# Optimization experiments

Hardware: AMD Instinct MI355X
Metric: run time of the kernel (lower is better)

The kernel has to match this reference:

```python
import jax, jax.numpy as jnp
import numpy as np

BG_CLASS = 3          # eval path drops argmax-class==3
NMS_THRESH = 0.2      # nms(rois, scores, 0.2)
IMG_SIZE = 512.0      # ClipBoxes to 512x512 image
NUM_CLASSES = 4


def _decode_boxes(rois, deltas):
    # BBoxTransform: std weights (0.1, 0.1, 0.2, 0.2), then clip to image
    w = rois[:, 2] - rois[:, 0]
    h = rois[:, 3] - rois[:, 1]
    cx = rois[:, 0] + 0.5 * w
    cy = rois[:, 1] + 0.5 * h
    dx = deltas[:, 0] * 0.1
    dy = deltas[:, 1] * 0.1
    dw = deltas[:, 2] * 0.2
    dh = deltas[:, 3] * 0.2
    pcx = cx + dx * w
    pcy = cy + dy * h
    pw = jnp.exp(dw) * w
    ph = jnp.exp(dh) * h
    boxes = jnp.stack([pcx - 0.5 * pw, pcy - 0.5 * ph,
                       pcx + 0.5 * pw, pcy + 0.5 * ph], axis=1)
    return jnp.clip(boxes, 0.0, IMG_SIZE)


def _iou_one_vs_all(box, boxes):
    x1 = jnp.maximum(box[0], boxes[:, 0])
    y1 = jnp.maximum(box[1], boxes[:, 1])
    x2 = jnp.minimum(box[2], boxes[:, 2])
    y2 = jnp.minimum(box[3], boxes[:, 3])
    inter = jnp.clip(x2 - x1, 0.0) * jnp.clip(y2 - y1, 0.0)
    area_a = (box[2] - box[0]) * (box[3] - box[1])
    area_b = (boxes[:, 2] - boxes[:, 0]) * (boxes[:, 3] - boxes[:, 1])
    return inter / (area_a + area_b - inter + 1e-8)


def _nms_keep_mask(boxes, scores, thresh):
    # Fixed-shape NMS: returns bool keep mask over the original ordering.
    N = boxes.shape[0]
    order = jnp.argsort(-scores)           # descending score
    b = boxes[order]
    idx = jnp.arange(N)

    def body(i, keep):
        iou = _iou_one_vs_all(b[i], b)
        suppress = (iou > thresh) & (idx > i)
        return jnp.where(keep[i], keep & ~suppress, keep)

    keep_sorted = jax.lax.fori_loop(0, N, body, jnp.ones((N,), dtype=bool))
    return jnp.zeros((N,), dtype=bool).at[order].set(keep_sorted)


def _head(f, rois, w6, b6, w7, b7, wc, bc, wr, br):
    # TwoMLPHead
    v = jax.nn.relu(f @ w6.T + b6)          # [N, 1024]
    v = jax.nn.relu(v @ w7.T + b7)          # [N, 1024]
    # FastRCNNPredictor
    c = v @ wc.T + bc                        # [N, num_classes]
    r = v @ wr.T + br                        # [N, num_classes*4]
    classes = jnp.argmax(c, axis=1)          # torch.max(x,1)[1]
    scores = jnp.max(c, axis=1)              # torch.max(x,1)[0]
    deltas = jnp.take_along_axis(r.reshape(-1, NUM_CLASSES, 4),
                                 classes[:, None, None], axis=1)[:, 0, :]
    boxes = _decode_boxes(rois, deltas)
    return scores, classes, boxes


def setup_inputs() -> dict:
    key = jax.random.key(0)
    ks = jax.random.split(key, 10)
    N, D, H = 8000, 12544, 1024
    f = jax.random.normal(ks[0], (N, D), dtype=jnp.float32)
    # valid xyxy ROIs inside 512x512
    xy = jax.random.uniform(ks[1], (N, 2), minval=0.0, maxval=380.0)
    wh = jax.random.uniform(ks[2], (N, 2), minval=20.0, maxval=120.0)
    rois = jnp.concatenate([xy, xy + wh], axis=1).astype(jnp.float32)
    w6 = jax.random.normal(ks[3], (H, D), dtype=jnp.float32) * 0.01
    b6 = jnp.zeros((H,), dtype=jnp.float32)
    w7 = jax.random.normal(ks[4], (H, H), dtype=jnp.float32) * 0.02
    b7 = jnp.zeros((H,), dtype=jnp.float32)
    wc = jax.random.normal(ks[5], (NUM_CLASSES, H), dtype=jnp.float32) * 0.02
    bc = jnp.zeros((NUM_CLASSES,), dtype=jnp.float32)
    wr = jax.random.normal(ks[6], (NUM_CLASSES * 4, H), dtype=jnp.float32) * 0.02
    br = jnp.zeros((NUM_CLASSES * 4,), dtype=jnp.float32)
    return {"f": f, "rois": rois, "w6": w6, "b6": b6, "w7": w7, "b7": b7,
            "wc": wc, "bc": bc, "wr": wr, "br": br}


def reference(f, rois, w6, b6, w7, b7, wc, bc, wr, br):
    scores, classes, boxes = _head(f, rois, w6, b6, w7, b7, wc, bc, wr, br)
    valid = classes != BG_CLASS
    s_masked = jnp.where(valid, scores, -jnp.inf)
    keep = _nms_keep_mask(boxes, s_masked, NMS_THRESH) & valid
    # fixed-shape equivalent of (scores[index], labels[index], bboxes[index])
    return scores, classes, boxes, keep
```

## Files before the change

### kernel.cpp

```cpp
#include <hip/hip_runtime.h>
#include <hip/hip_fp16.h>
#include <math.h>

typedef _Float16 f16;
typedef _Float16 f16x2 __attribute__((ext_vector_type(2)));
typedef _Float16 f16x4 __attribute__((ext_vector_type(4)));
typedef _Float16 f16x8 __attribute__((ext_vector_type(8)));
typedef float f32x4 __attribute__((ext_vector_type(4)));
typedef unsigned long long u64;

#define GLD16(g, s) __builtin_amdgcn_global_load_lds( \
    (const __attribute__((address_space(1))) void*)(g), \
    (__attribute__((address_space(3))) void*)(s), 16, 0, 0)

struct HL { f16 h, l; };
__device__ __forceinline__ HL split1(float e) {
  float em = __uint_as_float(__float_as_uint(e) & 0xFFFFE000u);
  HL r;
  r.h = (f16)em;
  r.l = (f16)(e - em);
  return r;
}

__device__ __forceinline__ void splitcvt8(f32x4 u, f32x4 v, f16x8& H, f16x8& L) {
  union { f16x2 h2[4]; f16x8 h8; } uh, ul;
#pragma unroll
  for (int p = 0; p < 2; ++p) {
    float a = u[2 * p] * 256.0f, b = u[2 * p + 1] * 256.0f;
    float am = __uint_as_float(__float_as_uint(a) & 0xFFFFE000u);
    float bm = __uint_as_float(__float_as_uint(b) & 0xFFFFE000u);
    auto pk = __builtin_amdgcn_cvt_pkrtz(am, bm);
    uh.h2[p] = *reinterpret_cast<f16x2*>(&pk);
    auto pl = __builtin_amdgcn_cvt_pkrtz(a - am, b - bm);
    ul.h2[p] = *reinterpret_cast<f16x2*>(&pl);
  }
#pragma unroll
  for (int p = 0; p < 2; ++p) {
    float a = v[2 * p] * 256.0f, b = v[2 * p + 1] * 256.0f;
    float am = __uint_as_float(__float_as_uint(a) & 0xFFFFE000u);
    float bm = __uint_as_float(__float_as_uint(b) & 0xFFFFE000u);
    auto pk = __builtin_amdgcn_cvt_pkrtz(am, bm);
    uh.h2[2 + p] = *reinterpret_cast<f16x2*>(&pk);
    auto pl = __builtin_amdgcn_cvt_pkrtz(a - am, b - bm);
    ul.h2[2 + p] = *reinterpret_cast<f16x2*>(&pl);
  }
  H = uh.h8;
  L = ul.h8;
}

__global__ __launch_bounds__(256) void split_kernel(const float* __restrict__ src,
                                                    f16* __restrict__ hi,
                                                    f16* __restrict__ lo,
                                                    long n4, float scale) {
  long stride = (long)gridDim.x * blockDim.x;
  for (long i = (long)blockIdx.x * blockDim.x + threadIdx.x; i < n4; i += stride) {
    float4 v = ((const float4*)src)[i];
    f16x4 h, l;
    HL r0 = split1(v.x * scale); h[0] = r0.h; l[0] = r0.l;
    HL r1 = split1(v.y * scale); h[1] = r1.h; l[1] = r1.l;
    HL r2 = split1(v.z * scale); h[2] = r2.h; l[2] = r2.l;
    HL r3 = split1(v.w * scale); h[3] = r3.h; l[3] = r3.l;
    ((f16x4*)hi)[i] = h;
    ((f16x4*)lo)[i] = l;
  }
}

__global__ __launch_bounds__(256) void gemm1_128(
    const float* __restrict__ Af,
    const f16* __restrict__ B1, const f16* __restrict__ B2,
    const float* __restrict__ bias,
    f16* __restrict__ out1, f16* __restrict__ out2,
    const int M, const int K) {
  __shared__ __align__(16) char smem[2][32768];
  const int tid = threadIdx.x;
  const int lane = tid & 63;
  const int wid = tid >> 6;
  const int wr = wid >> 1, wcol = wid & 1;
  const int m0 = blockIdx.y * 128;
  const int n0 = blockIdx.x * 128;

  f32x4 acc[4][4];
#pragma unroll
  for (int m = 0; m < 4; ++m)
#pragma unroll
    for (int n = 0; n < 4; ++n) acc[m][n] = (f32x4){0.f, 0.f, 0.f, 0.f};

  const float* gAf[4];
#pragma unroll
  for (int q = 0; q < 4; ++q) {
    int rowg = m0 + q * 32 + (tid >> 3);
    if (rowg > M - 1) rowg = M - 1;
    const int chunkg = (tid & 7) ^ ((tid >> 3) & 7);
    gAf[q] = Af + (size_t)rowg * K + chunkg * 4;
  }
  const int rq = tid >> 2;
  const int cg = (((tid & 3) ^ ((rq >> 1) & 3)) * 8);
  const f16* gB1q0 = B1 + (size_t)(n0 + rq) * K + cg;
  const f16* gB1q1 = B1 + (size_t)(n0 + 64 + rq) * K + cg;
  const f16* gB2q0 = B2 + (size_t)(n0 + rq) * K + cg;
  const f16* gB2q1 = B2 + (size_t)(n0 + 64 + rq) * K + cg;
  const int du = wid * 512;

  const int arow = wr * 64 + (lane & 15);
  const int brow = wcol * 64 + (lane & 15);
  const int kcB = (((lane >> 4) ^ ((brow >> 1) & 3)) * 8);
  const int pA0 = (((lane >> 4) * 2)     ^ (arow & 7)) * 4;
  const int pA1 = (((lane >> 4) * 2 + 1) ^ (arow & 7)) * 4;

  const int nt = K / 32;

#define STAGE(buf, kt)                                            \
  do {                                                            \
    char* smx_ = smem[buf];                                       \
    float* db = (float*)smx_;                                     \
    GLD16(gAf[0] + (kt), db + 0 * 1024 + wid * 256);              \
    GLD16(gAf[1] + (kt), db + 1 * 1024 + wid * 256);              \
    GLD16(gAf[2] + (kt), db + 2 * 1024 + wid * 256);              \
    GLD16(gAf[3] + (kt), db + 3 * 1024 + wid * 256);              \
    GLD16(gB1q0 + (kt), (f16*)(smx_ + 16384) + du);               \
    GLD16(gB1q1 + (kt), (f16*)(smx_ + 16384) + 2048 + du);        \
    GLD16(gB2q0 + (kt), (f16*)(smx_ + 24576) + du);               \
    GLD16(gB2q1 + (kt), (f16*)(smx_ + 24576) + 2048 + du);        \
  } while (0)

  STAGE(0, 0);

  for (int t = 0; t < nt; ++t) {
    asm volatile("s_waitcnt vmcnt(0)" ::: "memory");
    asm volatile("s_waitcnt lgkmcnt(0)" ::: "memory");
    __builtin_amdgcn_s_barrier();
    __builtin_amdgcn_sched_barrier(0);

    const char* smx = smem[t & 1];
    const float* sf = (const float*)smx;
    f16x8 a1[4], a2[4], b1[4], b2[4];
#pragma unroll
    for (int m = 0; m < 4; ++m) {
      const float* rp = sf + (arow + m * 16) * 32;
      f32x4 u = *(const f32x4*)(rp + pA0);
      f32x4 v = *(const f32x4*)(rp + pA1);
      splitcvt8(u, v, a1[m], a2[m]);
    }
    {
      const f16* sb1 = (const f16*)(smx + 16384);
      const f16* sb2 = (const f16*)(smx + 24576);
#pragma unroll
      for (int n = 0; n < 4; ++n) {
        b1[n] = *(const f16x8*)&sb1[(brow + n * 16) * 32 + kcB];
        b2[n] = *(const f16x8*)&sb2[(brow + n * 16) * 32 + kcB];
      }
    }

    if (t + 1 < nt) STAGE((t + 1) & 1, (t + 1) * 32);

#pragma unroll
    for (int m = 0; m < 4; ++m)
#pragma unroll
      for (int n = 0; n < 4; ++n)
        acc[m][n] = __builtin_amdgcn_mfma_f32_16x16x32_f16(a1[m], b1[n], acc[m][n], 0, 0, 0);
#pragma unroll
    for (int m = 0; m < 4; ++m)
#pragma unroll
      for (int n = 0; n < 4; ++n)
        acc[m][n] = __builtin_amdgcn_mfma_f32_16x16x32_f16(a2[m], b1[n], acc[m][n], 0, 0, 0);
#pragma unroll
    for (int m = 0; m < 4; ++m)
#pragma unroll
      for (int n = 0; n < 4; ++n)
        acc[m][n] = __builtin_amdgcn_mfma_f32_16x16x32_f16(a1[m], b2[n], acc[m][n], 0, 0, 0);
  }
#undef STAGE

  const int crow = m0 + wr * 64 + 4 * (lane >> 4);
  const int ccol0 = n0 + wcol * 64 + (lane & 15);
#pragma unroll
  for (int n = 0; n < 4; ++n) {
    const int col = ccol0 + n * 16;
    const float bv = bias[col];
#pragma unroll
    for (int m = 0; m < 4; ++m) {
#pragma unroll
      for (int j = 0; j < 4; ++j) {
        const int row = crow + m * 16 + j;
        if (row < M) {
          float v = acc[m][n][j] * (1.0f / 65536.0f) + bv;
          v = fmaxf(v, 0.0f);
          HL r = split1(v * 256.0f);
          out1[(size_t)row * 1024 + col] = r.h;
          out2[(size_t)row * 1024 + col] = r.l;
        }
      }
    }
  }
}

__global__ __launch_bounds__(512) void gemm2_k(
    const f16* __restrict__ A1, const f16* __restrict__ A2,
    const f16* __restrict__ B1, const f16* __restrict__ B2,
    const float* __restrict__ bias,
    float* __restrict__ out1,
    const int M, const int K) {
  __shared__ __align__(16) char smem[3][49152];
  const int tid = threadIdx.x;
  const int lane = tid & 63;
  const int wid = tid >> 6;
  const int wr = wid >> 1, wcol = wid & 1;
  const int m0 = blockIdx.y * 256;
  const int n0 = blockIdx.x * 128;

  f32x4 acc[4][4];
#pragma unroll
  for (int m = 0; m < 4; ++m)
#pragma unroll
    for (int n = 0; n < 4; ++n) acc[m][n] = (f32x4){0.f, 0.f, 0.f, 0.f};

  const int cg = (((tid & 3) ^ ((tid >> 3) & 3)) * 8);
  const f16* gB1 = B1 + (size_t)(n0 + (tid >> 2)) * K + cg;
  const f16* gB2 = B2 + (size_t)(n0 + (tid >> 2)) * K + cg;
  int ra0 = m0 + (tid >> 2);       if (ra0 > M - 1) ra0 = M - 1;
  int ra1 = m0 + 128 + (tid >> 2); if (ra1 > M - 1) ra1 = M - 1;
  const f16* gA1q0 = A1 + (size_t)ra0 * K + cg;
  const f16* gA1q1 = A1 + (size_t)ra1 * K + cg;
  const f16* gA2q0 = A2 + (size_t)ra0 * K + cg;
  const f16* gA2q1 = A2 + (size_t)ra1 * K + cg;

  const int arow = wr * 64 + (lane & 15);
  const int brow = wcol * 64 + (lane & 15);
  const int kcA = (((lane >> 4) ^ ((arow >> 1) & 3)) * 8);
  const int kcB = (((lane >> 4) ^ ((brow >> 1) & 3)) * 8);

  const int nt = K / 32;

#define STAGE(buf, kt)                                            \
  do {                                                            \
    char* smx_ = smem[buf];                                       \
    f16* d1 = (f16*)smx_;                                         \
    f16* d2 = d1 + 8192;                                          \
    GLD16(gA1q0 + (kt), d1 + wid * 512);                          \
    GLD16(gA1q1 + (kt), d1 + 4096 + wid * 512);                   \
    GLD16(gA2q0 + (kt), d2 + wid * 512);                          \
    GLD16(gA2q1 + (kt), d2 + 4096 + wid * 512);                   \
    GLD16(gB1 + (kt), (f16*)(smx_ + 32768) + wid * 512);          \
    GLD16(gB2 + (kt), (f16*)(smx_ + 40960) + wid * 512);          \
  } while (0)

  STAGE(0, 0);
  if (nt > 1) STAGE(1, 32);
  int cur = 0;

  for (int t = 0; t < nt; ++t) {
    if (t + 1 < nt) asm volatile("s_waitcnt vmcnt(6)" ::: "memory");
    else            asm volatile("s_waitcnt vmcnt(0)" ::: "memory");
    asm volatile("s_waitcnt lgkmcnt(0)" ::: "memory");
    __builtin_amdgcn_s_barrier();
    __builtin_amdgcn_sched_barrier(0);

    const char* smx = smem[cur];
    const f16* s1 = (const f16*)smx;
    const f16* s2 = s1 + 8192;
    const f16* sb1 = (const f16*)(smx + 32768);
    const f16* sb2 = (const f16*)(smx + 40960);
    f16x8 a1[4], a2[4], b1[4], b2[4];
#pragma unroll
    for (int m = 0; m < 4; ++m) {
      a1[m] = *(const f16x8*)&s1[(arow + m * 16) * 32 + kcA];
      a2[m] = *(const f16x8*)&s2[(arow + m * 16) * 32 + kcA];
    }
#pragma unroll
    for (int n = 0; n < 4; ++n) {
      b1[n] = *(const f16x8*)&sb1[(brow + n * 16) * 32 + kcB];
      b2[n] = *(const f16x8*)&sb2[(brow + n * 16) * 32 + kcB];
    }

    int pre = cur + 2; if (pre >= 3) pre -= 3;
    if (t + 2 < nt) STAGE(pre, (t + 2) * 32);

#pragma unroll
    for (int m = 0; m < 4; ++m)
#pragma unroll
      for (int n = 0; n < 4; ++n)
        acc[m][n] = __builtin_amdgcn_mfma_f32_16x16x32_f16(a1[m], b1[n], acc[m][n], 0, 0, 0);
#pragma unroll
    for (int m = 0; m < 4; ++m)
#pragma unroll
      for (int n = 0; n < 4; ++n)
        acc[m][n] = __builtin_amdgcn_mfma_f32_16x16x32_f16(a2[m], b1[n], acc[m][n], 0, 0, 0);
#pragma unroll
    for (int m = 0; m < 4; ++m)
#pragma unroll
      for (int n = 0; n < 4; ++n)
        acc[m][n] = __builtin_amdgcn_mfma_f32_16x16x32_f16(a1[m], b2[n], acc[m][n], 0, 0, 0);

    ++cur; if (cur >= 3) cur = 0;
  }
#undef STAGE

  const int crow = m0 + wr * 64 + 4 * (lane >> 4);
  const int ccol0 = n0 + wcol * 64 + (lane & 15);
#pragma unroll
  for (int n = 0; n < 4; ++n) {
    const int col = ccol0 + n * 16;
    const float bv = bias[col];
#pragma unroll
    for (int m = 0; m < 4; ++m) {
#pragma unroll
      for (int j = 0; j < 4; ++j) {
        const int row = crow + m * 16 + j;
        if (row < M) {
          float v = acc[m][n][j] * (1.0f / 65536.0f) + bv;
          out1[(size_t)row * 1024 + col] = fmaxf(v, 0.0f);
        }
      }
    }
  }
}

__device__ __forceinline__ float dot4f(float4 a, float4 b) {
  return a.x * b.x + a.y * b.y + a.z * b.z + a.w * b.w;
}

__global__ __launch_bounds__(256) void head_final(
    const float* __restrict__ v7,
    const float* __restrict__ wc, const float* __restrict__ bc,
    const float* __restrict__ wr, const float* __restrict__ br,
    const float* __restrict__ rois,
    float* __restrict__ outScores, float* __restrict__ outClasses,
    float* __restrict__ outBoxes,
    float* __restrict__ smask, float* __restrict__ wsbox, int* __restrict__ wsval) {
  const int gw = (blockIdx.x * 256 + threadIdx.x) >> 6;
  const int lane = threadIdx.x & 63;
  if (gw >= 8000) return;

  const float4* vr = (const float4*)(v7 + (size_t)gw * 1024);
  float4 x0 = vr[lane], x1 = vr[64 + lane], x2 = vr[128 + lane], x3 = vr[192 + lane];

  float s[20];
#pragma unroll
  for (int o = 0; o < 20; ++o) {
    const float* wrow = (o < 4) ? (wc + o * 1024) : (wr + (o - 4) * 1024);
    const float4* w4 = (const float4*)wrow;
    float a = dot4f(x0, w4[lane]) + dot4f(x1, w4[64 + lane]) +
              dot4f(x2, w4[128 + lane]) + dot4f(x3, w4[192 + lane]);
#pragma unroll
    for (int off = 32; off >= 1; off >>= 1) a += __shfl_xor(a, off);
    s[o] = a + ((o < 4) ? bc[o] : br[o - 4]);
  }

  float best = s[0]; int cls = 0;
  if (s[1] > best) { best = s[1]; cls = 1; }
  if (s[2] > best) { best = s[2]; cls = 2; }
  if (s[3] > best) { best = s[3]; cls = 3; }

  float d0, d1, d2, d3;
  if      (cls == 0) { d0 = s[4];  d1 = s[5];  d2 = s[6];  d3 = s[7];  }
  else if (cls == 1) { d0 = s[8];  d1 = s[9];  d2 = s[10]; d3 = s[11]; }
  else if (cls == 2) { d0 = s[12]; d1 = s[13]; d2 = s[14]; d3 = s[15]; }
  else               { d0 = s[16]; d1 = s[17]; d2 = s[18]; d3 = s[19]; }

  float4 rb = ((const float4*)rois)[gw];
  float w = rb.z - rb.x, h = rb.w - rb.y;
  float cx = rb.x + 0.5f * w, cy = rb.y + 0.5f * h;
  float pcx = cx + d0 * 0.1f * w;
  float pcy = cy + d1 * 0.1f * h;
  float pw = expf(d2 * 0.2f) * w;
  float ph = expf(d3 * 0.2f) * h;
  float bx0 = fminf(fmaxf(pcx - 0.5f * pw, 0.f), 512.f);
  float by0 = fminf(fmaxf(pcy - 0.5f * ph, 0.f), 512.f);
  float bx1 = fminf(fmaxf(pcx + 0.5f * pw, 0.f), 512.f);
  float by1 = fminf(fmaxf(pcy + 0.5f * ph, 0.f), 512.f);

  if (lane == 0) {
    outScores[gw] = best;
    outClasses[gw] = (float)cls;
    outBoxes[gw * 4 + 0] = bx0;
    outBoxes[gw * 4 + 1] = by0;
    outBoxes[gw * 4 + 2] = bx1;
    outBoxes[gw * 4 + 3] = by1;
    int valid = (cls != 3);
    smask[gw] = valid ? best : -INFINITY;
    wsval[gw] = valid;
    float4 bb; bb.x = bx0; bb.y = by0; bb.z = bx1; bb.w = by1;
    ((float4*)wsbox)[gw] = bb;
  }
}

__global__ __launch_bounds__(256) void rank_kernel(
    const float* __restrict__ smask, const float* __restrict__ bx,
    const int* __restrict__ valid,
    int* __restrict__ order, float* __restrict__ sboxes, int* __restrict__ svalid) {
  __shared__ __align__(16) float sS[8000];
  const int tid = threadIdx.x;
  for (int i = tid; i < 8000; i += 256) sS[i] = smask[i];
  __syncthreads();
  const int i = blockIdx.x * 256 + tid;
  if (i >= 8000) return;
  const float si = sS[i];
  int cnt = 0;
  const float4* s4p = (const float4*)sS;
  for (int j4 = 0; j4 < 2000; j4 += 4) {
    float4 sa = s4p[j4], sb = s4p[j4 + 1], sc = s4p[j4 + 2], sd = s4p[j4 + 3];
    int jb = j4 * 4;
    cnt += (sa.x > si) || (sa.x == si && (jb + 0) < i);
    cnt += (sa.y > si) || (sa.y == si && (jb + 1) < i);
    cnt += (sa.z > si) || (sa.z == si && (jb + 2) < i);
    cnt += (sa.w > si) || (sa.w == si && (jb + 3) < i);
    cnt += (sb.x > si) || (sb.x == si && (jb + 4) < i);
    cnt += (sb.y > si) || (sb.y == si && (jb + 5) < i);
    cnt += (sb.z > si) || (sb.z == si && (jb + 6) < i);
    cnt += (sb.w > si) || (sb.w == si && (jb + 7) < i);
    cnt += (sc.x > si) || (sc.x == si && (jb + 8) < i);
    cnt += (sc.y > si) || (sc.y == si && (jb + 9) < i);
    cnt += (sc.z > si) || (sc.z == si && (jb + 10) < i);
    cnt += (sc.w > si) || (sc.w == si && (jb + 11) < i);
    cnt += (sd.x > si) || (sd.x == si && (jb + 12) < i);
    cnt += (sd.y > si) || (sd.y == si && (jb + 13) < i);
    cnt += (sd.z > si) || (sd.z == si && (jb + 14) < i);
    cnt += (sd.w > si) || (sd.w == si && (jb + 15) < i);
  }
  order[cnt] = i;
  svalid[cnt] = valid[i];
  ((float4*)sboxes)[cnt] = ((const float4*)bx)[i];
}

__global__ __launch_bounds__(256) void iou_matrix(const float* __restrict__ sboxes,
                                                  u64* __restrict__ M,
                                                  u64* __restrict__ Mdiag,
                                                  const int* __restrict__ svalid) {
  const int t = blockIdx.y;
  const int w = blockIdx.x * 4 + (threadIdx.x >> 6);
  if (w < t || w >= 125) return;
  if (svalid[t * 64] == 0 || svalid[w * 64] == 0) return;
  const int lane = threadIdx.x & 63;
  const int ri = t * 64 + lane;
  float4 rb = ((const float4*)sboxes)[ri];
  const float ra = (rb.z - rb.x) * (rb.w - rb.y);
  const float4* cb = (const float4*)sboxes + w * 64;
  u64 bits = 0;
#pragma unroll 4
  for (int j = 0; j < 64; ++j) {
    float4 c = cb[j];
    float x1 = fmaxf(rb.x, c.x), y1 = fmaxf(rb.y, c.y);
    float x2 = fminf(rb.z, c.z), y2 = fminf(rb.w, c.w);
    float inter = fmaxf(x2 - x1, 0.f) * fmaxf(y2 - y1, 0.f);
    float ca = (c.z - c.x) * (c.w - c.y);
    float iou = inter / (ra + ca - inter + 1e-8f);
    int gc = w * 64 + j;
    if (iou > 0.2f && gc > ri) bits |= (1ULL << j);
  }
  M[(size_t)ri * 128 + w] = bits;
  if (w == t) Mdiag[(size_t)t * 64 + lane] = bits;
}

__global__ __launch_bounds__(128) void nms_scan(
    const u64* __restrict__ M, const u64* __restrict__ Mdiag,
    const int* __restrict__ order,
    const int* __restrict__ svalid, float* __restrict__ outKeep) {
  __shared__ __align__(16) u64 sMdiag[8000];
  __shared__ u64 acc[126];
  __shared__ unsigned char klist[64];
  __shared__ int kcount;
  __shared__ int tv[125];
  __shared__ int nvt_s;
  const int tid = threadIdx.x;
  for (int i = tid; i < 4000; i += 128)
    ((float4*)sMdiag)[i] = ((const float4*)Mdiag)[i];
  for (int w = tid; w < 125; w += 128) acc[w] = 0;
  if (tid < 125) tv[tid] = svalid[tid * 64];
  __syncthreads();
  if (tid == 0) {
    int c = 0;
    while (c < 125 && tv[c]) ++c;
    nvt_s = c;
  }
  __syncthreads();
  const int nvt = nvt_s;

  for (int t = 0; t < nvt; ++t) {
    if (tid < 64) {
      u64 myrow = sMdiag[t * 64 + tid];
      unsigned mlo = (unsigned)myrow, mhi = (unsigned)(myrow >> 32);
      u64 r = acc[t];
      u64 rem = ~r;
      while (rem) {
        int i = __builtin_ctzll(rem);
        unsigned rlo = (unsigned)__builtin_amdgcn_readlane((int)mlo, i);
        unsigned rhi = (unsigned)__builtin_amdgcn_readlane((int)mhi, i);
        u64 rowi = ((u64)rhi << 32) | (u64)rlo;
        r |= rowi;
        rem &= ~(rowi | (1ULL << i));
      }
      u64 kept = ~r;
      if (tid == 0) { acc[t] = r; kcount = (int)__popcll(kept); }
      if ((kept >> tid) & 1ULL)
        klist[__popcll(kept & ((1ULL << tid) - 1ULL))] = (unsigned char)tid;
    }
    __syncthreads();
    const int kc = kcount;
    const int w = t + 1 + tid;
    if (w < nvt) {
      u64 a = acc[w];
      const u64* base = M + (size_t)t * 64 * 128 + w;
      int j = 0;
      for (; j + 16 <= kc; j += 16) {
        u64 o = 0;
#pragma unroll
        for (int q = 0; q < 16; ++q) o |= base[(size_t)klist[j + q] * 128];
        a |= o;
      }
      for (; j + 4 <= kc; j += 4) {
        u64 v0 = base[(size_t)klist[j] * 128];
        u64 v1 = base[(size_t)klist[j + 1] * 128];
        u64 v2 = base[(size_t)klist[j + 2] * 128];
        u64 v3 = base[(size_t)klist[j + 3] * 128];
        a |= (v0 | v1) | (v2 | v3);
      }
      for (; j < kc; ++j) a |= base[(size_t)klist[j] * 128];
      acc[w] = a;
    }
    __syncthreads();
  }

  for (int p = tid; p < 8000; p += 128) {
    int removed = (int)((acc[p >> 6] >> (p & 63)) & 1ULL);
    float kv = (!removed && svalid[p]) ? 1.0f : 0.0f;
    outKeep[order[p]] = kv;
  }
}

extern "C" void kernel_launch(void* const* d_in, const int* in_sizes, int n_in,
                              void* d_out, int out_size, void* d_ws, size_t ws_size,
                              hipStream_t stream) {
  const float* F    = (const float*)d_in[0];
  const float* ROIS = (const float*)d_in[1];
  const float* W6   = (const float*)d_in[2];
  const float* B6   = (const float*)d_in[3];
  const float* W7   = (const float*)d_in[4];
  const float* B7   = (const float*)d_in[5];
  const float* WC   = (const float*)d_in[6];
  const float* BC   = (const float*)d_in[7];
  const float* WR   = (const float*)d_in[8];
  const float* BR   = (const float*)d_in[9];

  const size_t N = 8000, D = 12544, H = 1024;
  char* ws = (char*)d_ws;
  size_t off = 0;
  auto alloc = [&](size_t bytes) -> void* {
    void* p = (void*)(ws + off);
    off += (bytes + 255) & ~(size_t)255;
    return p;
  };
  f16*   B1w   = (f16*)alloc(H * D * 2);
  f16*   B2w   = (f16*)alloc(H * D * 2);
  f16*   V61   = (f16*)alloc(N * H * 2);
  f16*   V62   = (f16*)alloc(N * H * 2);
  f16*   W71   = (f16*)alloc(H * H * 2);
  f16*   W72   = (f16*)alloc(H * H * 2);
  float* V7    = (float*)alloc(N * H * 4);
  float* SMASK = (float*)alloc(N * 4);
  float* WSBOX = (float*)alloc(N * 16);
  int*   WSVAL = (int*)alloc(N * 4);
  int*   ORDER = (int*)alloc(N * 4);
  float* SBOX  = (float*)alloc(N * 16);
  int*   SVAL  = (int*)alloc(N * 4);
  u64*   MM    = (u64*)alloc(N * 128 * 8);
  u64*   MDIAG = (u64*)alloc(125 * 64 * 8);

  float* outScores  = (float*)d_out;
  float* outClasses = (float*)d_out + 8000;
  float* outBoxes   = (float*)d_out + 16000;
  float* outKeep    = (float*)d_out + 48000;

  split_kernel<<<1024, 256, 0, stream>>>(W6, B1w, B2w, (long)(H * D / 4), 256.0f);
  split_kernel<<<256, 256, 0, stream>>>(W7, W71, W72, (long)(H * H / 4), 256.0f);

  gemm1_128<<<dim3(8, 63), 256, 0, stream>>>(F, B1w, B2w, B6, V61, V62, 8000, 12544);
  gemm2_k<<<dim3(8, 32), 512, 0, stream>>>(V61, V62, W71, W72, B7, V7, 8000, 1024);

  head_final<<<2000, 256, 0, stream>>>(V7, WC, BC, WR, BR, ROIS,
                                       outScores, outClasses, outBoxes,
                                       SMASK, WSBOX, WSVAL);
  rank_kernel<<<32, 256, 0, stream>>>(SMASK, WSBOX, WSVAL, ORDER, SBOX, SVAL);
  iou_matrix<<<dim3(32, 125), 256, 0, stream>>>(SBOX, MM, MDIAG, SVAL);
  nms_scan<<<1, 128, 0, stream>>>(MM, MDIAG, ORDER, SVAL, outKeep);
}
```

Before: 1.153 ms.

## Parallelize score ranking across wavefront lanes with shuffle reduction

Each score's rank is now computed by a whole 64-lane wavefront instead of a single thread, with lanes striding over the scores and combining counts via xor shuffles. The grid grows from 32 blocks to 2000 to fill all compute units. The LDS load is vectorized with float4. The trade-off is that every block reloads the full score array into LDS, adding redundant global/L2 traffic.

```diff
diff --git a/kernel.cpp b/kernel.cpp
--- a/kernel.cpp
+++ b/kernel.cpp
@@ -390,36 +390,26 @@
     int* __restrict__ order, float* __restrict__ sboxes, int* __restrict__ svalid) {
   __shared__ __align__(16) float sS[8000];
   const int tid = threadIdx.x;
-  for (int i = tid; i < 8000; i += 256) sS[i] = smask[i];
+  for (int i = tid; i < 2000; i += 256)
+    ((float4*)sS)[i] = ((const float4*)smask)[i];
   __syncthreads();
-  const int i = blockIdx.x * 256 + tid;
-  if (i >= 8000) return;
+  const int i = blockIdx.x * 4 + (tid >> 6);
+  const int lane = tid & 63;
   const float si = sS[i];
   int cnt = 0;
-  const float4* s4p = (const float4*)sS;
-  for (int j4 = 0; j4 < 2000; j4 += 4) {
-    float4 sa = s4p[j4], sb = s4p[j4 + 1], sc = s4p[j4 + 2], sd = s4p[j4 + 3];
-    int jb = j4 * 4;
-    cnt += (sa.x > si) || (sa.x == si && (jb + 0) < i);
-    cnt += (sa.y > si) || (sa.y == si && (jb + 1) < i);
-    cnt += (sa.z > si) || (sa.z == si && (jb + 2) < i);
-    cnt += (sa.w > si) || (sa.w == si && (jb + 3) < i);
-    cnt += (sb.x > si) || (sb.x == si && (jb + 4) < i);
-    cnt += (sb.y > si) || (sb.y == si && (jb + 5) < i);
-    cnt += (sb.z > si) || (sb.z == si && (jb + 6) < i);
-    cnt += (sb.w > si) || (sb.w == si && (jb + 7) < i);
-    cnt += (sc.x > si) || (sc.x == si && (jb + 8) < i);
-    cnt += (sc.y > si) || (sc.y == si && (jb + 9) < i);
-    cnt += (sc.z > si) || (sc.z == si && (jb + 10) < i);
-    cnt += (sc.w > si) || (sc.w == si && (jb + 11) < i);
-    cnt += (sd.x > si) || (sd.x == si && (jb + 12) < i);
-    cnt += (sd.y > si) || (sd.y == si && (jb + 13) < i);
-    cnt += (sd.z > si) || (sd.z == si && (jb + 14) < i);
-    cnt += (sd.w > si) || (sd.w == si && (jb + 15) < i);
-  }
-  order[cnt] = i;
-  svalid[cnt] = valid[i];
-  ((float4*)sboxes)[cnt] = ((const float4*)bx)[i];
+#pragma unroll 5
+  for (int k = 0; k < 125; ++k) {
+    const int j = k * 64 + lane;
+    const float sj = sS[j];
+    cnt += (sj > si) || (sj == si && j < i);
+  }
+#pragma unroll
+  for (int off = 32; off >= 1; off >>= 1) cnt += __shfl_xor(cnt, off);
+  if (lane == 0) {
+    order[cnt] = i;
+    svalid[cnt] = valid[i];
+    ((float4*)sboxes)[cnt] = ((const float4*)bx)[i];
+  }
 }
 
 __global__ __launch_bounds__(256) void iou_matrix(const float* __restrict__ sboxes,
@@ -579,7 +569,7 @@
   head_final<<<2000, 256, 0, stream>>>(V7, WC, BC, WR, BR, ROIS,
                                        outScores, outClasses, outBoxes,
                                        SMASK, WSBOX, WSVAL);
-  rank_kernel<<<32, 256, 0, stream>>>(SMASK, WSBOX, WSVAL, ORDER, SBOX, SVAL);
+  rank_kernel<<<2000, 256, 0, stream>>>(SMASK, WSBOX, WSVAL, ORDER, SBOX, SVAL);
   iou_matrix<<<dim3(32, 125), 256, 0, stream>>>(SBOX, MM, MDIAG, SVAL);
   nms_scan<<<1, 128, 0, stream>>>(MM, MDIAG, ORDER, SVAL, outKeep);
 }
```

Measured after the change: 941.8 us. 1.22x faster.
